# Optimization experiments

Measured on AMD Instinct MI355X. Metric: run time of the kernel, lower is better.

Reference implementation:

```python
import jax, jax.numpy as jnp
import numpy as np

TAU = 0.8
N, D = 4096, 512

def _proj(x, W, b):
    # nn.Linear then ELU (torch Linear: x @ W.T + b)
    return jax.nn.elu(x @ W.T + b)

def setup_inputs() -> dict:
    key = jax.random.key(0)
    k1, k2, k3, k4, k5 = jax.random.split(key, 5)
    v1 = jax.random.normal(k1, (N, D), dtype=jnp.float32)
    v2 = jax.random.normal(k2, (N, D), dtype=jnp.float32)
    pos = jax.random.uniform(k3, (N, N), dtype=jnp.float32)
    neg = jax.random.uniform(k4, (N, N), dtype=jnp.float32)
    W = jax.random.normal(k5, (D, D), dtype=jnp.float32) * (1.414 / np.sqrt(D))
    b = jnp.zeros((D,), dtype=jnp.float32)
    return {"v1_embs": v1, "v2_embs": v2, "pos": pos, "neg": neg, "W_proj": W, "b_proj": b}

def reference(v1_embs, v2_embs, pos, neg, W_proj, b_proj):
    z1 = _proj(v1_embs, W_proj, b_proj)
    z2 = _proj(v2_embs, W_proj, b_proj)
    # cosine-similarity style: dot / (|z1||z2|) / tau, then exp
    n1 = jnp.linalg.norm(z1, axis=-1, keepdims=True)  # [N,1]
    n2 = jnp.linalg.norm(z2, axis=-1, keepdims=True)  # [N,1]
    dots = z1 @ z2.T                                   # [N,N]
    sim = jnp.exp(dots / (n1 * n2.T) / TAU)
    sim_pos = sim * pos
    sim_neg = sim * neg
    ratio = sim_pos.sum() / (sim_pos + sim_neg).sum()
    return -jnp.log(ratio)
```

## Files before the change

kernel.cpp:

```cpp
#include <hip/hip_runtime.h>
#include <hip/hip_bf16.h>
#include <math.h>

#define NROWS 4096
#define DDIM  512
#define INV_TAU 1.25f
#define SROW 132

typedef __attribute__((ext_vector_type(8))) short short8;
typedef __attribute__((ext_vector_type(4))) float f32x4;

__device__ inline void gload_lds16(const void* g, void* l) {
  __builtin_amdgcn_global_load_lds(
      (const __attribute__((address_space(1))) void*)g,
      (__attribute__((address_space(3))) void*)l, 16, 0, 0);
}

__device__ inline unsigned short f2bf(float f) {
  __hip_bfloat16 h = __float2bfloat16(f);
  return __builtin_bit_cast(unsigned short, h);
}
__device__ inline float bf2f(unsigned short u) {
  return __bfloat162float(__builtin_bit_cast(__hip_bfloat16, u));
}

__global__ void convert_kernel(const float* __restrict__ v1,
                               const float* __restrict__ v2,
                               const float* __restrict__ W,
                               unsigned short* __restrict__ v1b,
                               unsigned short* __restrict__ v2b,
                               unsigned short* __restrict__ Wb,
                               float* __restrict__ nsq1,
                               float* __restrict__ nsq2) {
  int idx = blockIdx.x * blockDim.x + threadIdx.x;
  if (idx < NROWS) { nsq1[idx] = 0.f; nsq2[idx] = 0.f; }
  const int TOTV = (NROWS * DDIM) / 4;
  const int TOTW = (DDIM * DDIM) / 4;
  const int total = 2 * TOTV + TOTW;
  const int stride = gridDim.x * blockDim.x;
  for (int i = idx; i < total; i += stride) {
    const float4* src; unsigned short* dst; int j;
    if (i < TOTV)            { src = (const float4*)v1; dst = v1b; j = i; }
    else if (i < 2 * TOTV)   { src = (const float4*)v2; dst = v2b; j = i - TOTV; }
    else                     { src = (const float4*)W;  dst = Wb;  j = i - 2 * TOTV; }
    float4 x = src[j];
    ushort4 o;
    o.x = f2bf(x.x); o.y = f2bf(x.y); o.z = f2bf(x.z); o.w = f2bf(x.w);
    *(ushort4*)&dst[j * 4] = o;
  }
}

__global__ __launch_bounds__(256) void proj_kernel(
    const unsigned short* __restrict__ v1b, const unsigned short* __restrict__ v2b,
    const unsigned short* __restrict__ Wb,  const float* __restrict__ bias,
    unsigned short* __restrict__ z1b, unsigned short* __restrict__ z2b,
    float* __restrict__ nsq1, float* __restrict__ nsq2) {
  __shared__ __align__(16) unsigned short As[128 * 32];
  __shared__ __align__(16) unsigned short Bs[128 * 32];
  const int tid = threadIdx.x;
  const int wid = tid >> 6, lane = tid & 63;
  const int wm = wid >> 1, wn = wid & 1;
  const int l15 = lane & 15, l4 = lane >> 4;

  const int zsel = blockIdx.z;
  const unsigned short* Ag = (zsel ? v2b : v1b) + (size_t)blockIdx.y * 128 * DDIM;
  const unsigned short* Bg = Wb + (size_t)blockIdx.x * 128 * DDIM;
  unsigned short* Z = (zsel ? z2b : z1b);
  float* nsq = (zsel ? nsq2 : nsq1);

  f32x4 acc[4][4];
#pragma unroll
  for (int m = 0; m < 4; ++m)
#pragma unroll
    for (int n = 0; n < 4; ++n) acc[m][n] = (f32x4){0.f, 0.f, 0.f, 0.f};

  for (int kt = 0; kt < DDIM; kt += 32) {
#pragma unroll
    for (int i = 0; i < 2; ++i) {
      int off = i * 4096 + tid * 16;
      int row = off >> 6;
      int kb  = off & 63;
      gload_lds16((const char*)(Ag + row * DDIM + kt) + kb,
                  (char*)As + i * 4096 + wid * 1024);
      gload_lds16((const char*)(Bg + row * DDIM + kt) + kb,
                  (char*)Bs + i * 4096 + wid * 1024);
    }
    asm volatile("s_waitcnt vmcnt(0)" ::: "memory");
    __syncthreads();
    short8 av[4], bv[4];
#pragma unroll
    for (int m = 0; m < 4; ++m)
      av[m] = *(const short8*)&As[(wm * 64 + m * 16 + l15) * 32 + l4 * 8];
#pragma unroll
    for (int n = 0; n < 4; ++n)
      bv[n] = *(const short8*)&Bs[(wn * 64 + n * 16 + l15) * 32 + l4 * 8];
#pragma unroll
    for (int m = 0; m < 4; ++m)
#pragma unroll
      for (int n = 0; n < 4; ++n)
        acc[m][n] = __builtin_amdgcn_mfma_f32_16x16x32_bf16(
            av[m], bv[n], acc[m][n], 0, 0, 0);
    __syncthreads();
  }

  const int rowBase = blockIdx.y * 128 + wm * 64;
  const int colBase = blockIdx.x * 128 + wn * 64;
  float bcol[4];
#pragma unroll
  for (int n = 0; n < 4; ++n) bcol[n] = bias[colBase + n * 16 + l15];
#pragma unroll
  for (int m = 0; m < 4; ++m) {
#pragma unroll
    for (int reg = 0; reg < 4; ++reg) {
      int gRow = rowBase + m * 16 + l4 * 4 + reg;
      float rs = 0.f;
#pragma unroll
      for (int n = 0; n < 4; ++n) {
        int gCol = colBase + n * 16 + l15;
        float y = acc[m][n][reg] + bcol[n];
        float zv = (y > 0.f) ? y : expm1f(y);
        unsigned short zb = f2bf(zv);
        Z[(size_t)gRow * DDIM + gCol] = zb;
        float zf = bf2f(zb);
        rs += zf * zf;
      }
      rs += __shfl_xor(rs, 1, 64);
      rs += __shfl_xor(rs, 2, 64);
      rs += __shfl_xor(rs, 4, 64);
      rs += __shfl_xor(rs, 8, 64);
      if (l15 == 0) atomicAdd(&nsq[gRow], rs);
    }
  }
}

__global__ __launch_bounds__(256, 4) void dots_kernel(
    const unsigned short* __restrict__ z1b, const unsigned short* __restrict__ z2b,
    const float* __restrict__ nsq1, const float* __restrict__ nsq2,
    const float* __restrict__ pos, const float* __restrict__ neg,
    double* __restrict__ partials) {
  __shared__ __align__(16) char smem[2][16384];
  float* sCh = (float*)smem;

  const int tid = threadIdx.x;
  const int wid = tid >> 6, lane = tid & 63;
  const int wm = wid >> 1, wn = wid & 1;
  const int l15 = lane & 15, l4 = lane >> 4;

  const int bid = blockIdx.x;
  const int by = bid >> 5, bx = bid & 31;

  const unsigned short* Ag = z1b + (size_t)by * 128 * DDIM;
  const unsigned short* Bg = z2b + (size_t)bx * 128 * DDIM;

  f32x4 acc[4][4];
#pragma unroll
  for (int m = 0; m < 4; ++m)
#pragma unroll
    for (int n = 0; n < 4; ++n) acc[m][n] = (f32x4){0.f, 0.f, 0.f, 0.f};

#define STAGE(buf, t)                                                          \
  {                                                                            \
    _Pragma("unroll")                                                          \
    for (int i = 0; i < 2; ++i) {                                              \
      int off = i * 4096 + tid * 16;                                           \
      int row = off >> 6;                                 \
      int gsw = ((off >> 4) & 3) ^ ((row >> 1) & 3);                           \
      gload_lds16((const char*)Ag + row * 1024 + (t) * 64 + gsw * 16,          \
                  smem[buf] + i * 4096 + wid * 1024);                          \
      gload_lds16((const char*)Bg + row * 1024 + (t) * 64 + gsw * 16,          \
                  smem[buf] + 8192 + i * 4096 + wid * 1024);                   \
    }                                                                          \
  }

  STAGE(0, 0);
  STAGE(1, 1);

  const int aswz = (l4 ^ ((l15 >> 1) & 3)) * 8;

#pragma unroll
  for (int t = 0; t < 16; ++t) {
    if (t < 15) asm volatile("s_waitcnt vmcnt(4)" ::: "memory");
    else        asm volatile("s_waitcnt vmcnt(0)" ::: "memory");
    __builtin_amdgcn_s_barrier();
    const unsigned short* As = (const unsigned short*)smem[t & 1];
    const unsigned short* Bs = (const unsigned short*)(smem[t & 1] + 8192);
    short8 av[4], bv[4];
#pragma unroll
    for (int m = 0; m < 4; ++m)
      av[m] = *(const short8*)&As[(wm * 64 + m * 16 + l15) * 32 + aswz];
#pragma unroll
    for (int n = 0; n < 4; ++n)
      bv[n] = *(const short8*)&Bs[(wn * 64 + n * 16 + l15) * 32 + aswz];
#pragma unroll
    for (int m = 0; m < 4; ++m)
#pragma unroll
      for (int n = 0; n < 4; ++n)
        acc[m][n] = __builtin_amdgcn_mfma_f32_16x16x32_bf16(
            av[m], bv[n], acc[m][n], 0, 0, 0);
    __builtin_amdgcn_s_barrier();
    if (t < 14) STAGE(t & 1, t + 2);
  }
#undef STAGE

  const int blockRow = by * 128;
  const int blockCol = bx * 128;
  const int rowBase = blockRow + wm * 64;
  const int colBase = blockCol + wn * 64;

  float rs2[4];
#pragma unroll
  for (int n = 0; n < 4; ++n) rs2[n] = rsqrtf(nsq2[colBase + n * 16 + l15]);

  const int lr = tid >> 3;
  const int lcBase = (tid & 7) * 16;
  const int gRowRbase = blockRow + (lr >> 4) * 64 + (lr & 15);
  const int lrW = wm * 16 + l4 * 4;
  const int lcW = wn * 64 + l15;

  float sumP = 0.f, sumT = 0.f;
#pragma unroll
  for (int m = 0; m < 4; ++m) {
    const float* pr = pos + (size_t)(gRowRbase + m * 16) * NROWS + blockCol + lcBase;
    const float* gr = neg + (size_t)(gRowRbase + m * 16) * NROWS + blockCol + lcBase;
    float4 pv[4], gv[4];
#pragma unroll
    for (int i = 0; i < 4; ++i) {
      pv[i] = *(const float4*)(pr + 4 * i);
      gv[i] = *(const float4*)(gr + 4 * i);
    }
#pragma unroll
    for (int reg = 0; reg < 4; ++reg) {
      float rs1 = rsqrtf(nsq1[rowBase + m * 16 + l4 * 4 + reg]);
#pragma unroll
      for (int n = 0; n < 4; ++n) {
        float s = __expf(acc[m][n][reg] * (rs1 * rs2[n]) * INV_TAU);
        sCh[(lrW + reg) * SROW + lcW + n * 16] = s;
      }
    }
    __syncthreads();
#pragma unroll
    for (int i = 0; i < 4; ++i) {
      float4 s4 = *(const float4*)&sCh[lr * SROW + lcBase + 4 * i];
      sumP += s4.x * pv[i].x + s4.y * pv[i].y + s4.z * pv[i].z + s4.w * pv[i].w;
      sumT += s4.x * (pv[i].x + gv[i].x) + s4.y * (pv[i].y + gv[i].y) +
              s4.z * (pv[i].z + gv[i].z) + s4.w * (pv[i].w + gv[i].w);
    }
    __syncthreads();
  }

#pragma unroll
  for (int sft = 1; sft < 64; sft <<= 1) {
    sumP += __shfl_xor(sumP, sft, 64);
    sumT += __shfl_xor(sumT, sft, 64);
  }
  __shared__ float redP[4], redT[4];
  if (lane == 0) { redP[wid] = sumP; redT[wid] = sumT; }
  __syncthreads();
  if (tid == 0) {
    double tp = (double)redP[0] + redP[1] + redP[2] + redP[3];
    double tt = (double)redT[0] + redT[1] + redT[2] + redT[3];
    partials[2 * bid]     = tp;
    partials[2 * bid + 1] = tt;
  }
}

__global__ void finalize_kernel(const double* __restrict__ partials,
                                float* __restrict__ out) {
  __shared__ double sp[256], st[256];
  int t = threadIdx.x;
  double a = 0.0, b = 0.0;
  for (int i = t; i < 1024; i += 256) {
    a += partials[2 * i];
    b += partials[2 * i + 1];
  }
  sp[t] = a; st[t] = b;
  __syncthreads();
  for (int s = 128; s > 0; s >>= 1) {
    if (t < s) { sp[t] += sp[t + s]; st[t] += st[t + s]; }
    __syncthreads();
  }
  if (t == 0) out[0] = (float)(log(st[0]) - log(sp[0]));
}

extern "C" void kernel_launch(void* const* d_in, const int* in_sizes, int n_in,
                              void* d_out, int out_size, void* d_ws, size_t ws_size,
                              hipStream_t stream) {
  (void)in_sizes; (void)n_in; (void)out_size; (void)ws_size;
  const float* v1   = (const float*)d_in[0];
  const float* v2   = (const float*)d_in[1];
  const float* pos  = (const float*)d_in[2];
  const float* neg  = (const float*)d_in[3];
  const float* W    = (const float*)d_in[4];
  const float* bias = (const float*)d_in[5];

  char* ws = (char*)d_ws;
  unsigned short* z1b = (unsigned short*)(ws + 0);
  unsigned short* z2b = (unsigned short*)(ws + 4194304);
  unsigned short* v1b = (unsigned short*)(ws + 8388608);
  unsigned short* v2b = (unsigned short*)(ws + 12582912);
  unsigned short* Wb  = (unsigned short*)(ws + 16777216);
  float* nsq1         = (float*)(ws + 17301504);
  float* nsq2         = (float*)(ws + 17317888);
  double* partials    = (double*)(ws + 17334272);
  float* out = (float*)d_out;

  hipLaunchKernelGGL(convert_kernel, dim3(1024), dim3(256), 0, stream,
                     v1, v2, W, v1b, v2b, Wb, nsq1, nsq2);
  hipLaunchKernelGGL(proj_kernel, dim3(DDIM / 128, NROWS / 128, 2), dim3(256), 0, stream,
                     v1b, v2b, Wb, bias, z1b, z2b, nsq1, nsq2);
  hipLaunchKernelGGL(dots_kernel, dim3(1024), dim3(256), 0, stream,
                     z1b, z2b, nsq1, nsq2, pos, neg, partials);
  hipLaunchKernelGGL(finalize_kernel, dim3(1), dim3(256), 0, stream,
                     partials, out);
}
```

Before: 74.80 us.

## Enlarge dots kernel tiles to 256x256 with 512 threads and swizzled block order

Result: faster. 70.19 us (-6.2%).

```diff
diff --git a/kernel.cpp b/kernel.cpp
--- a/kernel.cpp
+++ b/kernel.cpp
@@ -5,7 +5,7 @@
 #define NROWS 4096
 #define DDIM  512
 #define INV_TAU 1.25f
-#define SROW 132
+#define SROW 260
 
 typedef __attribute__((ext_vector_type(8))) short short8;
 typedef __attribute__((ext_vector_type(4))) float f32x4;
@@ -133,28 +133,31 @@
   }
 }
 
-__global__ __launch_bounds__(256, 4) void dots_kernel(
+__global__ __launch_bounds__(512, 1) void dots_kernel(
     const unsigned short* __restrict__ z1b, const unsigned short* __restrict__ z2b,
     const float* __restrict__ nsq1, const float* __restrict__ nsq2,
     const float* __restrict__ pos, const float* __restrict__ neg,
     double* __restrict__ partials) {
-  __shared__ __align__(16) char smem[2][16384];
+  __shared__ __align__(16) char smem[2][32768];
   float* sCh = (float*)smem;
 
   const int tid = threadIdx.x;
   const int wid = tid >> 6, lane = tid & 63;
-  const int wm = wid >> 1, wn = wid & 1;
+  const int wm = wid >> 2, wn = wid & 3;
   const int l15 = lane & 15, l4 = lane >> 4;
 
   const int bid = blockIdx.x;
-  const int by = bid >> 5, bx = bid & 31;
-
-  const unsigned short* Ag = z1b + (size_t)by * 128 * DDIM;
-  const unsigned short* Bg = z2b + (size_t)bx * 128 * DDIM;
-
-  f32x4 acc[4][4];
-#pragma unroll
-  for (int m = 0; m < 4; ++m)
+  const int swz = (bid & 7) * 32 + (bid >> 3);
+  const int S = swz >> 5, s5 = swz & 31;
+  const int by = (S >> 1) * 4 + (s5 >> 3);
+  const int bx = (S & 1) * 8 + (s5 & 7);
+
+  const unsigned short* Ag = z1b + (size_t)by * 256 * DDIM;
+  const unsigned short* Bg = z2b + (size_t)bx * 256 * DDIM;
+
+  f32x4 acc[8][4];
+#pragma unroll
+  for (int m = 0; m < 8; ++m)
 #pragma unroll
     for (int n = 0; n < 4; ++n) acc[m][n] = (f32x4){0.f, 0.f, 0.f, 0.f};
 
@@ -162,13 +165,13 @@
   {                                                                            \
     _Pragma("unroll")                                                          \
     for (int i = 0; i < 2; ++i) {                                              \
-      int off = i * 4096 + tid * 16;                                           \
+      int off = i * 8192 + tid * 16;                                           \
       int row = off >> 6;                                 \
       int gsw = ((off >> 4) & 3) ^ ((row >> 1) & 3);                           \
       gload_lds16((const char*)Ag + row * 1024 + (t) * 64 + gsw * 16,          \
-                  smem[buf] + i * 4096 + wid * 1024);                          \
+                  smem[buf] + i * 8192 + wid * 1024);                          \
       gload_lds16((const char*)Bg + row * 1024 + (t) * 64 + gsw * 16,          \
-                  smem[buf] + 8192 + i * 4096 + wid * 1024);                   \
+                  smem[buf] + 16384 + i * 8192 + wid * 1024);                  \
     }                                                                          \
   }
 
@@ -183,16 +186,16 @@
     else        asm volatile("s_waitcnt vmcnt(0)" ::: "memory");
     __builtin_amdgcn_s_barrier();
     const unsigned short* As = (const unsigned short*)smem[t & 1];
-    const unsigned short* Bs = (const unsigned short*)(smem[t & 1] + 8192);
-    short8 av[4], bv[4];
-#pragma unroll
-    for (int m = 0; m < 4; ++m)
-      av[m] = *(const short8*)&As[(wm * 64 + m * 16 + l15) * 32 + aswz];
+    const unsigned short* Bs = (const unsigned short*)(smem[t & 1] + 16384);
+    short8 av[8], bv[4];
+#pragma unroll
+    for (int m = 0; m < 8; ++m)
+      av[m] = *(const short8*)&As[(wm * 128 + m * 16 + l15) * 32 + aswz];
 #pragma unroll
     for (int n = 0; n < 4; ++n)
       bv[n] = *(const short8*)&Bs[(wn * 64 + n * 16 + l15) * 32 + aswz];
 #pragma unroll
-    for (int m = 0; m < 4; ++m)
+    for (int m = 0; m < 8; ++m)
 #pragma unroll
       for (int n = 0; n < 4; ++n)
         acc[m][n] = __builtin_amdgcn_mfma_f32_16x16x32_bf16(
@@ -202,26 +205,25 @@
   }
 #undef STAGE
 
-  const int blockRow = by * 128;
-  const int blockCol = bx * 128;
-  const int rowBase = blockRow + wm * 64;
-  const int colBase = blockCol + wn * 64;
+  const int blockRow = by * 256;
+  const int blockCol = bx * 256;
 
   float rs2[4];
 #pragma unroll
-  for (int n = 0; n < 4; ++n) rs2[n] = rsqrtf(nsq2[colBase + n * 16 + l15]);
-
-  const int lr = tid >> 3;
-  const int lcBase = (tid & 7) * 16;
-  const int gRowRbase = blockRow + (lr >> 4) * 64 + (lr & 15);
+  for (int n = 0; n < 4; ++n)
+    rs2[n] = rsqrtf(nsq2[blockCol + wn * 64 + n * 16 + l15]);
+
+  const int lr = tid >> 4;
+  const int lcBase = (tid & 15) * 16;
   const int lrW = wm * 16 + l4 * 4;
   const int lcW = wn * 64 + l15;
 
   float sumP = 0.f, sumT = 0.f;
 #pragma unroll
-  for (int m = 0; m < 4; ++m) {
-    const float* pr = pos + (size_t)(gRowRbase + m * 16) * NROWS + blockCol + lcBase;
-    const float* gr = neg + (size_t)(gRowRbase + m * 16) * NROWS + blockCol + lcBase;
+  for (int m = 0; m < 8; ++m) {
+    const int gRowR = blockRow + (lr >> 4) * 128 + m * 16 + (lr & 15);
+    const float* pr = pos + (size_t)gRowR * NROWS + blockCol + lcBase;
+    const float* gr = neg + (size_t)gRowR * NROWS + blockCol + lcBase;
     float4 pv[4], gv[4];
 #pragma unroll
     for (int i = 0; i < 4; ++i) {
@@ -230,11 +232,11 @@
     }
 #pragma unroll
     for (int reg = 0; reg < 4; ++reg) {
-      float rs1 = rsqrtf(nsq1[rowBase + m * 16 + l4 * 4 + reg]);
+      float rs1 = rsqrtf(nsq1[blockRow + wm * 128 + m * 16 + l4 * 4 + reg]);
 #pragma unroll
       for (int n = 0; n < 4; ++n) {
-        float s = __expf(acc[m][n][reg] * (rs1 * rs2[n]) * INV_TAU);
-        sCh[(lrW + reg) * SROW + lcW + n * 16] = s;
+        float ss = __expf(acc[m][n][reg] * (rs1 * rs2[n]) * INV_TAU);
+        sCh[(lrW + reg) * SROW + lcW + n * 16] = ss;
       }
     }
     __syncthreads();
@@ -253,12 +255,13 @@
     sumP += __shfl_xor(sumP, sft, 64);
     sumT += __shfl_xor(sumT, sft, 64);
   }
-  __shared__ float redP[4], redT[4];
+  __shared__ float redP[8], redT[8];
   if (lane == 0) { redP[wid] = sumP; redT[wid] = sumT; }
   __syncthreads();
   if (tid == 0) {
-    double tp = (double)redP[0] + redP[1] + redP[2] + redP[3];
-    double tt = (double)redT[0] + redT[1] + redT[2] + redT[3];
+    double tp = 0.0, tt = 0.0;
+#pragma unroll
+    for (int w = 0; w < 8; ++w) { tp += redP[w]; tt += redT[w]; }
     partials[2 * bid]     = tp;
     partials[2 * bid + 1] = tt;
   }
@@ -268,12 +271,8 @@
                                 float* __restrict__ out) {
   __shared__ double sp[256], st[256];
   int t = threadIdx.x;
-  double a = 0.0, b = 0.0;
-  for (int i = t; i < 1024; i += 256) {
-    a += partials[2 * i];
-    b += partials[2 * i + 1];
-  }
-  sp[t] = a; st[t] = b;
+  sp[t] = partials[2 * t];
+  st[t] = partials[2 * t + 1];
   __syncthreads();
   for (int s = 128; s > 0; s >>= 1) {
     if (t < s) { sp[t] += sp[t + s]; st[t] += st[t + s]; }
@@ -308,7 +307,7 @@
                      v1, v2, W, v1b, v2b, Wb, nsq1, nsq2);
   hipLaunchKernelGGL(proj_kernel, dim3(DDIM / 128, NROWS / 128, 2), dim3(256), 0, stream,
                      v1b, v2b, Wb, bias, z1b, z2b, nsq1, nsq2);
-  hipLaunchKernelGGL(dots_kernel, dim3(1024), dim3(256), 0, stream,
+  hipLaunchKernelGGL(dots_kernel, dim3(256), dim3(512), 0, stream,
                      z1b, z2b, nsq1, nsq2, pos, neg, partials);
   hipLaunchKernelGGL(finalize_kernel, dim3(1), dim3(256), 0, stream,
                      partials, out);
```

## Split fused dots/reduce into GEMM writing bf16 sim and a streaming reduce

Applied to the files above, without the earlier changes.

New measurement: 84.21 us. +12.6%, slower.

```diff
diff --git a/kernel.cpp b/kernel.cpp
--- a/kernel.cpp
+++ b/kernel.cpp
@@ -5,9 +5,9 @@
 #define NROWS 4096
 #define DDIM  512
 #define INV_TAU 1.25f
-#define SROW 132
 
 typedef __attribute__((ext_vector_type(8))) short short8;
+typedef __attribute__((ext_vector_type(8))) unsigned short ushort8;
 typedef __attribute__((ext_vector_type(4))) float f32x4;
 
 __device__ inline void gload_lds16(const void* g, void* l) {
@@ -133,7 +133,141 @@
   }
 }
 
-__global__ __launch_bounds__(256, 4) void dots_kernel(
+__global__ __launch_bounds__(256, 4) void dotsA_kernel(
+    const unsigned short* __restrict__ z1b, const unsigned short* __restrict__ z2b,
+    const float* __restrict__ nsq1, const float* __restrict__ nsq2,
+    unsigned short* __restrict__ sim) {
+  __shared__ __align__(16) char smem[2][16384];
+
+  const int tid = threadIdx.x;
+  const int wid = tid >> 6, lane = tid & 63;
+  const int wm = wid >> 1, wn = wid & 1;
+  const int l15 = lane & 15, l4 = lane >> 4;
+
+  const int bid = blockIdx.x;
+  const int by = bid >> 5, bx = bid & 31;
+
+  const unsigned short* Ag = z1b + (size_t)by * 128 * DDIM;
+  const unsigned short* Bg = z2b + (size_t)bx * 128 * DDIM;
+
+  f32x4 acc[4][4];
+#pragma unroll
+  for (int m = 0; m < 4; ++m)
+#pragma unroll
+    for (int n = 0; n < 4; ++n) acc[m][n] = (f32x4){0.f, 0.f, 0.f, 0.f};
+
+#define STAGE(buf, t)                                                          \
+  {                                                                            \
+    _Pragma("unroll")                                                          \
+    for (int i = 0; i < 2; ++i) {                                              \
+      int off = i * 4096 + tid * 16;                                           \
+      int row = off >> 6;                                                      \
+      int gsw = ((off >> 4) & 3) ^ ((row >> 1) & 3);                           \
+      gload_lds16((const char*)Ag + row * 1024 + (t) * 64 + gsw * 16,          \
+                  smem[buf] + i * 4096 + wid * 1024);                          \
+      gload_lds16((const char*)Bg + row * 1024 + (t) * 64 + gsw * 16,          \
+                  smem[buf] + 8192 + i * 4096 + wid * 1024);                   \
+    }                                                                          \
+  }
+
+  STAGE(0, 0);
+  STAGE(1, 1);
+
+  const int aswz = (l4 ^ ((l15 >> 1) & 3)) * 8;
+
+#pragma unroll
+  for (int t = 0; t < 16; ++t) {
+    if (t < 15) asm volatile("s_waitcnt vmcnt(4)" ::: "memory");
+    else        asm volatile("s_waitcnt vmcnt(0)" ::: "memory");
+    __builtin_amdgcn_s_barrier();
+    const unsigned short* As = (const unsigned short*)smem[t & 1];
+    const unsigned short* Bs = (const unsigned short*)(smem[t & 1] + 8192);
+    short8 av[4], bv[4];
+#pragma unroll
+    for (int m = 0; m < 4; ++m)
+      av[m] = *(const short8*)&As[(wm * 64 + m * 16 + l15) * 32 + aswz];
+#pragma unroll
+    for (int n = 0; n < 4; ++n)
+      bv[n] = *(const short8*)&Bs[(wn * 64 + n * 16 + l15) * 32 + aswz];
+#pragma unroll
+    for (int m = 0; m < 4; ++m)
+#pragma unroll
+      for (int n = 0; n < 4; ++n)
+        acc[m][n] = __builtin_amdgcn_mfma_f32_16x16x32_bf16(
+            av[m], bv[n], acc[m][n], 0, 0, 0);
+    __builtin_amdgcn_s_barrier();
+    if (t < 14) STAGE(t & 1, t + 2);
+  }
+#undef STAGE
+
+  const int rowBase = by * 128 + wm * 64;
+  const int colBase = bx * 128 + wn * 64;
+
+  float rs2[4], rs1[4][4];
+#pragma unroll
+  for (int n = 0; n < 4; ++n) rs2[n] = rsqrtf(nsq2[colBase + n * 16 + l15]);
+#pragma unroll
+  for (int m = 0; m < 4; ++m)
+#pragma unroll
+    for (int reg = 0; reg < 4; ++reg)
+      rs1[m][reg] = rsqrtf(nsq1[rowBase + m * 16 + l4 * 4 + reg]);
+
+#pragma unroll
+  for (int m = 0; m < 4; ++m)
+#pragma unroll
+    for (int reg = 0; reg < 4; ++reg) {
+      size_t rowOff = (size_t)(rowBase + m * 16 + l4 * 4 + reg) * NROWS;
+#pragma unroll
+      for (int n = 0; n < 4; ++n) {
+        float s = __expf(acc[m][n][reg] * (rs1[m][reg] * rs2[n]) * INV_TAU);
+        sim[rowOff + colBase + n * 16 + l15] = f2bf(s);
+      }
+    }
+}
+
+__global__ __launch_bounds__(256) void reduce_kernel(
+    const unsigned short* __restrict__ sim, const float* __restrict__ pos,
+    const float* __restrict__ neg, double* __restrict__ partials) {
+  const int tid = threadIdx.x;
+  const int gid = blockIdx.x * 256 + tid;
+  const int stride = 2048 * 256;
+  float sumP = 0.f, sumT = 0.f;
+#pragma unroll
+  for (int it = 0; it < 4; ++it) {
+    size_t base = ((size_t)(gid + it * stride)) * 8;
+    ushort8 sv = *(const ushort8*)(sim + base);
+    float4 p0 = *(const float4*)(pos + base);
+    float4 p1 = *(const float4*)(pos + base + 4);
+    float4 g0 = *(const float4*)(neg + base);
+    float4 g1 = *(const float4*)(neg + base + 4);
+    float s0 = bf2f(sv[0]), s1 = bf2f(sv[1]), s2 = bf2f(sv[2]), s3 = bf2f(sv[3]);
+    float s4 = bf2f(sv[4]), s5 = bf2f(sv[5]), s6 = bf2f(sv[6]), s7 = bf2f(sv[7]);
+    sumP += s0 * p0.x + s1 * p0.y + s2 * p0.z + s3 * p0.w +
+            s4 * p1.x + s5 * p1.y + s6 * p1.z + s7 * p1.w;
+    sumT += s0 * (p0.x + g0.x) + s1 * (p0.y + g0.y) +
+            s2 * (p0.z + g0.z) + s3 * (p0.w + g0.w) +
+            s4 * (p1.x + g1.x) + s5 * (p1.y + g1.y) +
+            s6 * (p1.z + g1.z) + s7 * (p1.w + g1.w);
+  }
+#pragma unroll
+  for (int sft = 1; sft < 64; sft <<= 1) {
+    sumP += __shfl_xor(sumP, sft, 64);
+    sumT += __shfl_xor(sumT, sft, 64);
+  }
+  __shared__ float redP[4], redT[4];
+  const int wid = tid >> 6;
+  if ((tid & 63) == 0) { redP[wid] = sumP; redT[wid] = sumT; }
+  __syncthreads();
+  if (tid == 0) {
+    double tp = (double)redP[0] + redP[1] + redP[2] + redP[3];
+    double tt = (double)redT[0] + redT[1] + redT[2] + redT[3];
+    partials[2 * blockIdx.x]     = tp;
+    partials[2 * blockIdx.x + 1] = tt;
+  }
+}
+
+#define SROW 132
+__global__ __launch_bounds__(256, 4) void dots_fused_kernel(
     const unsigned short* __restrict__ z1b, const unsigned short* __restrict__ z2b,
     const float* __restrict__ nsq1, const float* __restrict__ nsq2,
     const float* __restrict__ pos, const float* __restrict__ neg,
@@ -163,7 +297,7 @@
     _Pragma("unroll")                                                          \
     for (int i = 0; i < 2; ++i) {                                              \
       int off = i * 4096 + tid * 16;                                           \
-      int row = off >> 6;                                 \
+      int row = off >> 6;                                                      \
       int gsw = ((off >> 4) & 3) ^ ((row >> 1) & 3);                           \
       gload_lds16((const char*)Ag + row * 1024 + (t) * 64 + gsw * 16,          \
                   smem[buf] + i * 4096 + wid * 1024);                          \
@@ -174,7 +308,6 @@
 
   STAGE(0, 0);
   STAGE(1, 1);
-
   const int aswz = (l4 ^ ((l15 >> 1) & 3)) * 8;
 
 #pragma unroll
@@ -263,13 +396,14 @@
     partials[2 * bid + 1] = tt;
   }
 }
-
-__global__ void finalize_kernel(const double* __restrict__ partials,
+#undef SROW
+
+__global__ void finalize_kernel(const double* __restrict__ partials, int n,
                                 float* __restrict__ out) {
   __shared__ double sp[256], st[256];
   int t = threadIdx.x;
   double a = 0.0, b = 0.0;
-  for (int i = t; i < 1024; i += 256) {
+  for (int i = t; i < n; i += 256) {
     a += partials[2 * i];
     b += partials[2 * i + 1];
   }
@@ -285,7 +419,7 @@
 extern "C" void kernel_launch(void* const* d_in, const int* in_sizes, int n_in,
                               void* d_out, int out_size, void* d_ws, size_t ws_size,
                               hipStream_t stream) {
-  (void)in_sizes; (void)n_in; (void)out_size; (void)ws_size;
+  (void)in_sizes; (void)n_in; (void)out_size;
   const float* v1   = (const float*)d_in[0];
   const float* v2   = (const float*)d_in[1];
   const float* pos  = (const float*)d_in[2];
@@ -296,20 +430,31 @@
   char* ws = (char*)d_ws;
   unsigned short* z1b = (unsigned short*)(ws + 0);
   unsigned short* z2b = (unsigned short*)(ws + 4194304);
-  unsigned short* v1b = (unsigned short*)(ws + 8388608);
-  unsigned short* v2b = (unsigned short*)(ws + 12582912);
-  unsigned short* Wb  = (unsigned short*)(ws + 16777216);
-  float* nsq1         = (float*)(ws + 17301504);
-  float* nsq2         = (float*)(ws + 17317888);
-  double* partials    = (double*)(ws + 17334272);
+  float* nsq1         = (float*)(ws + 8388608);
+  float* nsq2         = (float*)(ws + 8404992);
+  double* partials    = (double*)(ws + 8421376);
+  unsigned short* v1b = (unsigned short*)(ws + 8453760);
+  unsigned short* v2b = (unsigned short*)(ws + 12648064);
+  unsigned short* Wb  = (unsigned short*)(ws + 16842368);
+  unsigned short* sim = (unsigned short*)(ws + 17366784);
+  const size_t NEED = 17366784 + (size_t)NROWS * NROWS * 2;
   float* out = (float*)d_out;
 
   hipLaunchKernelGGL(convert_kernel, dim3(1024), dim3(256), 0, stream,
                      v1, v2, W, v1b, v2b, Wb, nsq1, nsq2);
   hipLaunchKernelGGL(proj_kernel, dim3(DDIM / 128, NROWS / 128, 2), dim3(256), 0, stream,
                      v1b, v2b, Wb, bias, z1b, z2b, nsq1, nsq2);
-  hipLaunchKernelGGL(dots_kernel, dim3(1024), dim3(256), 0, stream,
-                     z1b, z2b, nsq1, nsq2, pos, neg, partials);
-  hipLaunchKernelGGL(finalize_kernel, dim3(1), dim3(256), 0, stream,
-                     partials, out);
-}
+  if (ws_size >= NEED) {
+    hipLaunchKernelGGL(dotsA_kernel, dim3(1024), dim3(256), 0, stream,
+                       z1b, z2b, nsq1, nsq2, sim);
+    hipLaunchKernelGGL(reduce_kernel, dim3(2048), dim3(256), 0, stream,
+                       sim, pos, neg, partials);
+    hipLaunchKernelGGL(finalize_kernel, dim3(1), dim3(256), 0, stream,
+                       partials, 2048, out);
+  } else {
+    hipLaunchKernelGGL(dots_fused_kernel, dim3(1024), dim3(256), 0, stream,
+                       z1b, z2b, nsq1, nsq2, pos, neg, partials);
+    hipLaunchKernelGGL(finalize_kernel, dim3(1), dim3(256), 0, stream,
+                       partials, 1024, out);
+  }
+}
```

## Split dots into FP8 sim materialization and separate pos/neg streaming reduction

Applied to the files above, without the earlier changes.

New measurement: 88.00 us. +17.7%, slower.

```diff
diff --git a/kernel.cpp b/kernel.cpp
--- a/kernel.cpp
+++ b/kernel.cpp
@@ -5,7 +5,6 @@
 #define NROWS 4096
 #define DDIM  512
 #define INV_TAU 1.25f
-#define SROW 132
 
 typedef __attribute__((ext_vector_type(8))) short short8;
 typedef __attribute__((ext_vector_type(4))) float f32x4;
@@ -22,6 +21,14 @@
 }
 __device__ inline float bf2f(unsigned short u) {
   return __bfloat162float(__builtin_bit_cast(__hip_bfloat16, u));
+}
+
+__device__ inline unsigned f2e4m3(float s) {
+  unsigned b = __builtin_bit_cast(unsigned, s);
+  return (b + 0x80000u - 0x3C000000u) >> 20;
+}
+__device__ inline float e4m32f(unsigned u8) {
+  return __builtin_bit_cast(float, (u8 << 20) + 0x3C000000u);
 }
 
 __global__ void convert_kernel(const float* __restrict__ v1,
@@ -133,13 +140,11 @@
   }
 }
 
-__global__ __launch_bounds__(256, 4) void dots_kernel(
+__global__ __launch_bounds__(256, 4) void dotsA_kernel(
     const unsigned short* __restrict__ z1b, const unsigned short* __restrict__ z2b,
     const float* __restrict__ nsq1, const float* __restrict__ nsq2,
-    const float* __restrict__ pos, const float* __restrict__ neg,
-    double* __restrict__ partials) {
+    unsigned char* __restrict__ sim) {
   __shared__ __align__(16) char smem[2][16384];
-  float* sCh = (float*)smem;
 
   const int tid = threadIdx.x;
   const int wid = tid >> 6, lane = tid & 63;
@@ -163,7 +168,7 @@
     _Pragma("unroll")                                                          \
     for (int i = 0; i < 2; ++i) {                                              \
       int off = i * 4096 + tid * 16;                                           \
-      int row = off >> 6;                                 \
+      int row = off >> 6;                                                      \
       int gsw = ((off >> 4) & 3) ^ ((row >> 1) & 3);                           \
       gload_lds16((const char*)Ag + row * 1024 + (t) * 64 + gsw * 16,          \
                   smem[buf] + i * 4096 + wid * 1024);                          \
@@ -202,74 +207,102 @@
   }
 #undef STAGE
 
-  const int blockRow = by * 128;
-  const int blockCol = bx * 128;
-  const int rowBase = blockRow + wm * 64;
-  const int colBase = blockCol + wn * 64;
-
-  float rs2[4];
+  const int rowBase = by * 128 + wm * 64;
+  const int colBase = bx * 128 + wn * 64;
+
+  float rs2[4], rs1[4][4];
 #pragma unroll
   for (int n = 0; n < 4; ++n) rs2[n] = rsqrtf(nsq2[colBase + n * 16 + l15]);
-
-  const int lr = tid >> 3;
-  const int lcBase = (tid & 7) * 16;
-  const int gRowRbase = blockRow + (lr >> 4) * 64 + (lr & 15);
-  const int lrW = wm * 16 + l4 * 4;
-  const int lcW = wn * 64 + l15;
-
-  float sumP = 0.f, sumT = 0.f;
-#pragma unroll
-  for (int m = 0; m < 4; ++m) {
-    const float* pr = pos + (size_t)(gRowRbase + m * 16) * NROWS + blockCol + lcBase;
-    const float* gr = neg + (size_t)(gRowRbase + m * 16) * NROWS + blockCol + lcBase;
-    float4 pv[4], gv[4];
-#pragma unroll
-    for (int i = 0; i < 4; ++i) {
-      pv[i] = *(const float4*)(pr + 4 * i);
-      gv[i] = *(const float4*)(gr + 4 * i);
-    }
+#pragma unroll
+  for (int m = 0; m < 4; ++m)
+#pragma unroll
+    for (int reg = 0; reg < 4; ++reg)
+      rs1[m][reg] = rsqrtf(nsq1[rowBase + m * 16 + l4 * 4 + reg]);
+
+  unsigned char* sB = (unsigned char*)smem;
+#pragma unroll
+  for (int m = 0; m < 4; ++m)
 #pragma unroll
     for (int reg = 0; reg < 4; ++reg) {
-      float rs1 = rsqrtf(nsq1[rowBase + m * 16 + l4 * 4 + reg]);
+      int lrow = wm * 64 + m * 16 + l4 * 4 + reg;
 #pragma unroll
       for (int n = 0; n < 4; ++n) {
-        float s = __expf(acc[m][n][reg] * (rs1 * rs2[n]) * INV_TAU);
-        sCh[(lrW + reg) * SROW + lcW + n * 16] = s;
+        float s = __expf(acc[m][n][reg] * (rs1[m][reg] * rs2[n]) * INV_TAU);
+        sB[lrow * 128 + wn * 64 + n * 16 + l15] = (unsigned char)f2e4m3(s);
       }
     }
-    __syncthreads();
-#pragma unroll
-    for (int i = 0; i < 4; ++i) {
-      float4 s4 = *(const float4*)&sCh[lr * SROW + lcBase + 4 * i];
-      sumP += s4.x * pv[i].x + s4.y * pv[i].y + s4.z * pv[i].z + s4.w * pv[i].w;
-      sumT += s4.x * (pv[i].x + gv[i].x) + s4.y * (pv[i].y + gv[i].y) +
-              s4.z * (pv[i].z + gv[i].z) + s4.w * (pv[i].w + gv[i].w);
-    }
-    __syncthreads();
-  }
+  __syncthreads();
+  {
+    int r = tid >> 1, h = tid & 1;
+    const uint4* src = (const uint4*)(sB + r * 128 + h * 64);
+    uint4 w0 = src[0], w1 = src[1], w2 = src[2], w3 = src[3];
+    uint4* dst = (uint4*)(sim + (size_t)(by * 128 + r) * NROWS + bx * 128 + h * 64);
+    dst[0] = w0; dst[1] = w1; dst[2] = w2; dst[3] = w3;
+  }
+}
+
+__global__ __launch_bounds__(256) void reduce_kernel(
+    const unsigned char* __restrict__ sim, const float* __restrict__ pos,
+    const float* __restrict__ neg, double* __restrict__ partials) {
+  const int tid = threadIdx.x;
+  const int gid = blockIdx.x * 256 + tid;
+  const int TOT = 4096 * 256;
+  const int gidN = (gid + TOT / 2) & (TOT - 1);
+
+  size_t bp0 = (size_t)gid * 8,          bp1 = (size_t)(gid + TOT) * 8;
+  size_t bg0 = (size_t)gidN * 8,         bg1 = (size_t)(gidN + TOT) * 8;
+
+  float4 p00 = *(const float4*)(pos + bp0);
+  float4 p01 = *(const float4*)(pos + bp0 + 4);
+  float4 p10 = *(const float4*)(pos + bp1);
+  float4 p11 = *(const float4*)(pos + bp1 + 4);
+  float4 g00 = *(const float4*)(neg + bg0);
+  float4 g01 = *(const float4*)(neg + bg0 + 4);
+  float4 g10 = *(const float4*)(neg + bg1);
+  float4 g11 = *(const float4*)(neg + bg1 + 4);
+  uint2  sp0 = *(const uint2*)(sim + bp0);
+  uint2  sp1 = *(const uint2*)(sim + bp1);
+  uint2  sg0 = *(const uint2*)(sim + bg0);
+  uint2  sg1 = *(const uint2*)(sim + bg1);
+
+  float sumP = 0.f, sumG = 0.f;
+#define ACC8(dst, sv, a, b)                                                    \
+  {                                                                            \
+    unsigned lo = sv.x, hi = sv.y;                                             \
+    dst += e4m32f((lo      ) & 0x7Fu) * a.x + e4m32f((lo >>  8) & 0x7Fu) * a.y \
+         + e4m32f((lo >> 16) & 0x7Fu) * a.z + e4m32f((lo >> 24) & 0x7Fu) * a.w \
+         + e4m32f((hi      ) & 0x7Fu) * b.x + e4m32f((hi >>  8) & 0x7Fu) * b.y \
+         + e4m32f((hi >> 16) & 0x7Fu) * b.z + e4m32f((hi >> 24) & 0x7Fu) * b.w;\
+  }
+  ACC8(sumP, sp0, p00, p01);
+  ACC8(sumP, sp1, p10, p11);
+  ACC8(sumG, sg0, g00, g01);
+  ACC8(sumG, sg1, g10, g11);
+#undef ACC8
 
 #pragma unroll
   for (int sft = 1; sft < 64; sft <<= 1) {
     sumP += __shfl_xor(sumP, sft, 64);
-    sumT += __shfl_xor(sumT, sft, 64);
-  }
-  __shared__ float redP[4], redT[4];
-  if (lane == 0) { redP[wid] = sumP; redT[wid] = sumT; }
+    sumG += __shfl_xor(sumG, sft, 64);
+  }
+  __shared__ float redP[4], redG[4];
+  const int wid = tid >> 6;
+  if ((tid & 63) == 0) { redP[wid] = sumP; redG[wid] = sumG; }
   __syncthreads();
   if (tid == 0) {
     double tp = (double)redP[0] + redP[1] + redP[2] + redP[3];
-    double tt = (double)redT[0] + redT[1] + redT[2] + redT[3];
-    partials[2 * bid]     = tp;
-    partials[2 * bid + 1] = tt;
-  }
-}
-
-__global__ void finalize_kernel(const double* __restrict__ partials,
+    double tg = (double)redG[0] + redG[1] + redG[2] + redG[3];
+    partials[2 * blockIdx.x]     = tp;
+    partials[2 * blockIdx.x + 1] = tp + tg;
+  }
+}
+
+__global__ void finalize_kernel(const double* __restrict__ partials, int n,
                                 float* __restrict__ out) {
   __shared__ double sp[256], st[256];
   int t = threadIdx.x;
   double a = 0.0, b = 0.0;
-  for (int i = t; i < 1024; i += 256) {
+  for (int i = t; i < n; i += 256) {
     a += partials[2 * i];
     b += partials[2 * i + 1];
   }
@@ -296,20 +329,23 @@
   char* ws = (char*)d_ws;
   unsigned short* z1b = (unsigned short*)(ws + 0);
   unsigned short* z2b = (unsigned short*)(ws + 4194304);
-  unsigned short* v1b = (unsigned short*)(ws + 8388608);
-  unsigned short* v2b = (unsigned short*)(ws + 12582912);
-  unsigned short* Wb  = (unsigned short*)(ws + 16777216);
-  float* nsq1         = (float*)(ws + 17301504);
-  float* nsq2         = (float*)(ws + 17317888);
-  double* partials    = (double*)(ws + 17334272);
+  float* nsq1         = (float*)(ws + 8388608);
+  float* nsq2         = (float*)(ws + 8404992);
+  double* partials    = (double*)(ws + 8421376);
+  unsigned short* v1b = (unsigned short*)(ws + 8486912);
+  unsigned short* v2b = (unsigned short*)(ws + 12681216);
+  unsigned short* Wb  = (unsigned short*)(ws + 16875520);
+  unsigned char*  sim = (unsigned char*)(ws + 17399808);
   float* out = (float*)d_out;
 
   hipLaunchKernelGGL(convert_kernel, dim3(1024), dim3(256), 0, stream,
                      v1, v2, W, v1b, v2b, Wb, nsq1, nsq2);
   hipLaunchKernelGGL(proj_kernel, dim3(DDIM / 128, NROWS / 128, 2), dim3(256), 0, stream,
                      v1b, v2b, Wb, bias, z1b, z2b, nsq1, nsq2);
-  hipLaunchKernelGGL(dots_kernel, dim3(1024), dim3(256), 0, stream,
-                     z1b, z2b, nsq1, nsq2, pos, neg, partials);
+  hipLaunchKernelGGL(dotsA_kernel, dim3(1024), dim3(256), 0, stream,
+                     z1b, z2b, nsq1, nsq2, sim);
+  hipLaunchKernelGGL(reduce_kernel, dim3(4096), dim3(256), 0, stream,
+                     sim, pos, neg, partials);
   hipLaunchKernelGGL(finalize_kernel, dim3(1), dim3(256), 0, stream,
-                     partials, out);
-}
+                     partials, 4096, out);
+}
```
